# Kernel optimization log

Measured on AMD Instinct MI355X. Metric: run time of the kernel, lower is better.

## Reference

```python
import jax, jax.numpy as jnp
import numpy as np

B, S, E, H = 4, 2048, 1024, 16
D = E // H  # head_dim = 64


def setup_inputs() -> dict:
    key = jax.random.key(0)
    k1, k2, k3 = jax.random.split(key, 3)
    x = jax.random.normal(k1, (B, S, E), dtype=jnp.float32)
    w_attn = jax.random.normal(k2, (E, 3 * E), dtype=jnp.float32) * (E ** -0.5)
    b_attn = jnp.zeros((3 * E,), dtype=jnp.float32)
    w_out = jax.random.normal(k3, (E, E), dtype=jnp.float32) * (E ** -0.5)
    b_out = jnp.zeros((E,), dtype=jnp.float32)
    return {"x": x, "w_attn": w_attn, "b_attn": b_attn, "w_out": w_out, "b_out": b_out}


def reference(x, w_attn, b_attn, w_out, b_out):
    b, s, e = x.shape
    qkv = x @ w_attn + b_attn                      # [b, s, 3e]
    q, k, v = jnp.split(qkv, 3, axis=2)
    q = q.reshape(b, s, H, D)
    k = k.reshape(b, s, H, D)
    v = v.reshape(b, s, H, D)
    energy = jnp.einsum('nqhd,nkhd->nhqk', q, k)   # [b, H, s, s]
    causal = jnp.tril(jnp.ones((s, s), dtype=bool))
    energy = jnp.where(causal, energy, -jnp.inf)
    scale = jnp.sqrt(jnp.float32(D))
    attn = jax.nn.softmax(energy / scale, axis=-1)  # dropout_rate=0.0 -> identity
    out = jnp.einsum('nhql,nlhd->nqhd', attn, v).reshape(b, s, e)
    return out @ w_out + b_out
```

## Files before the change

kernel.cpp:

```cpp
#include <hip/hip_runtime.h>

typedef short bf16x8 __attribute__((ext_vector_type(8)));
typedef float f32x4 __attribute__((ext_vector_type(4)));
typedef float f32x16 __attribute__((ext_vector_type(16)));
typedef float float4v __attribute__((ext_vector_type(4)));
typedef short short4v __attribute__((ext_vector_type(4)));
typedef unsigned uint2v __attribute__((ext_vector_type(2)));
typedef unsigned uint4v __attribute__((ext_vector_type(4)));

#define B_ 4
#define S_ 2048
#define E_ 1024
#define H_ 16
#define D_ 64
#define M_ (B_*S_)
#define N1_ (3*E_)

__device__ inline short f2bs(float f) {
    unsigned u = __builtin_bit_cast(unsigned, f);
    unsigned r = u + 0x7fffu + ((u >> 16) & 1u);
    return (short)(r >> 16);
}
__device__ inline float exp2a(float x) {
    float r; asm("v_exp_f32 %0, %1" : "=v"(r) : "v"(x)); return r;
}
__device__ inline unsigned cvtpk(float a, float b) {
    unsigned r; asm("v_cvt_pk_bf16_f32 %0, %1, %2" : "=v"(r) : "v"(a), "v"(b)); return r;
}

__device__ inline const __attribute__((address_space(1))) void* gas(const void* p) {
    return (const __attribute__((address_space(1))) void*)p;
}
__device__ inline __attribute__((address_space(3))) void* las(void* p) {
    return (__attribute__((address_space(3))) void*)p;
}

__global__ __launch_bounds__(256) void prologue(
    const float* __restrict__ x, short* __restrict__ Xbf,
    const float* __restrict__ w_attn, short* __restrict__ Wat,
    const float* __restrict__ w_out, short* __restrict__ Wot) {
    __shared__ float t[32][33];
    const int bid = blockIdx.x;
    const int tid = threadIdx.x;
    if (bid < 2048) {
        const int n = M_ * E_;
        const int stride = 2048 * 256 * 4;
        for (int i = (bid * 256 + tid) * 4; i < n; i += stride) {
            float4v v = *(const float4v*)&x[i];
            short4v o;
            o[0] = f2bs(v[0]); o[1] = f2bs(v[1]); o[2] = f2bs(v[2]); o[3] = f2bs(v[3]);
            *(short4v*)&Xbf[i] = o;
        }
    } else {
        const float* in;
        short* out;
        int rows, cols, bx, by;
        if (bid < 5120) {
            in = w_attn; out = Wat; rows = E_; cols = N1_;
            int b2 = bid - 2048;
            bx = (b2 % 96) * 32; by = (b2 / 96) * 32;
        } else {
            in = w_out; out = Wot; rows = E_; cols = E_;
            int b2 = bid - 5120;
            bx = (b2 & 31) * 32; by = (b2 >> 5) * 32;
        }
        const int tx = tid & 31, ty = tid >> 5;
#pragma unroll
        for (int i = 0; i < 4; ++i)
            t[ty + i * 8][tx] = in[(size_t)(by + ty + i * 8) * cols + bx + tx];
        __syncthreads();
#pragma unroll
        for (int i = 0; i < 4; ++i)
            out[(size_t)(bx + ty + i * 8) * rows + by + tx] = f2bs(t[tx][ty + i * 8]);
    }
}

#define VMW(n) asm volatile("s_waitcnt vmcnt(" #n ")" ::: "memory")
#define NOP_ ((void)0)

#define QKV_MFMA1(Q, AF) \
    _Pragma("unroll") for (int nf = 0; nf < 6; ++nf) { \
        acc[(Q)][nf] = __builtin_amdgcn_mfma_f32_16x16x32_bf16(AF[0], bfrag[nf][0], acc[(Q)][nf], 0, 0, 0); \
        acc[(Q)][nf] = __builtin_amdgcn_mfma_f32_16x16x32_bf16(AF[1], bfrag[nf][1], acc[(Q)][nf], 0, 0, 0); \
    }

#define QKV_PHASE2(QA, STAGE_STMT, WAITV) do { \
    bf16x8 afA[2], afB[2]; \
    const char* lA0 = lA + (QA) * 4096; \
    const char* lA1 = lA + ((QA) + 1) * 4096; \
    _Pragma("unroll") for (int ks = 0; ks < 2; ++ks) { \
        afA[ks] = *(const bf16x8*)(lA0 + li * 128 + ((ks * 64 + g * 16) ^ ((li & 7) << 4))); \
        afB[ks] = *(const bf16x8*)(lA1 + li * 128 + ((ks * 64 + g * 16) ^ ((li & 7) << 4))); \
    } \
    STAGE_STMT; \
    __builtin_amdgcn_s_barrier(); \
    asm volatile("s_waitcnt lgkmcnt(0)" ::: "memory"); \
    __builtin_amdgcn_sched_barrier(0); \
    __builtin_amdgcn_s_setprio(1); \
    QKV_MFMA1(QA, afA); \
    QKV_MFMA1((QA) + 1, afB); \
    __builtin_amdgcn_s_setprio(0); \
    WAITV; \
    __builtin_amdgcn_s_barrier(); \
} while (0)

__global__ __launch_bounds__(256, 2) void gemm_qkv(
    const short* __restrict__ A, const short* __restrict__ Bt,
    const float* __restrict__ bias,
    short* __restrict__ Qb, short* __restrict__ Kb, short* __restrict__ Vt) {
    __shared__ __attribute__((aligned(16))) short ldsA[2][8192];
    __shared__ __attribute__((aligned(16))) short ldsB[2][12288];
    const int tid = threadIdx.x;
    const int lane = tid & 63;
    const int wid = tid >> 6;
    const int li = lane & 15, g = lane >> 4;
    const int wr = wid >> 1, wc = wid & 1;
    const int Kdim = E_;
    const int NT = Kdim >> 6;

    const int id = blockIdx.x;
    const int swz = (id & 7) * 128 + (id >> 3);
    const int bx = swz & 15, by = swz >> 4;
    const int row0 = by * 128, col0 = bx * 192;

    const int lr8 = lane >> 3;
    const int cstage = (((lane & 7) ^ (lr8 & 7)) << 4);

    auto stageA = [&](int buf, int kt) {
#pragma unroll
        for (int Q = 0; Q < 4; ++Q) {
            int grow = (wid >> 1) * 64 + Q * 16 + (wid & 1) * 8 + lr8;
            const char* src = (const char*)A +
                ((size_t)(row0 + grow) * Kdim + kt * 64) * 2 + cstage;
            char* dst = (char*)&ldsA[buf][0] + Q * 4096 + wid * 1024;
            __builtin_amdgcn_global_load_lds(gas(src), las(dst), 16, 0, 0);
        }
    };
    auto stageB = [&](int buf, int kt) {
#pragma unroll
        for (int i = 0; i < 6; ++i) {
            int grow = i * 32 + wid * 8 + lr8;
            const char* src = (const char*)Bt +
                ((size_t)(col0 + grow) * Kdim + kt * 64) * 2 + cstage;
            char* dst = (char*)&ldsB[buf][0] + i * 4096 + wid * 1024;
            __builtin_amdgcn_global_load_lds(gas(src), las(dst), 16, 0, 0);
        }
    };

    f32x4 acc[4][6];
#pragma unroll
    for (int m = 0; m < 4; ++m)
#pragma unroll
        for (int n = 0; n < 6; ++n) acc[m][n] = (f32x4){0.f, 0.f, 0.f, 0.f};

    stageB(0, 0);
    stageA(0, 0);
    asm volatile("s_waitcnt vmcnt(0)" ::: "memory");
    __syncthreads();

    for (int t = 0; t < NT; ++t) {
        const int cur = t & 1;
        const int nb = cur ^ 1;
        const int tn = t + 1;
        const bool st = (tn < NT);
        const char* lA = (const char*)&ldsA[cur][0] + wr * 2048;
        const char* lB = (const char*)&ldsB[cur][0];

        bf16x8 bfrag[6][2];
#pragma unroll
        for (int nf = 0; nf < 6; ++nf)
#pragma unroll
            for (int ks = 0; ks < 2; ++ks) {
                int r = wc * 96 + nf * 16 + li;
                bfrag[nf][ks] = *(const bf16x8*)(lB + r * 128 + ((ks * 64 + g * 16) ^ ((r & 7) << 4)));
            }
        if (st) {
            QKV_PHASE2(0, stageB(nb, tn), VMW(6));
            QKV_PHASE2(2, stageA(nb, tn), VMW(2));
        } else {
            QKV_PHASE2(0, NOP_, VMW(0));
            QKV_PHASE2(2, NOP_, NOP_);
        }
    }

#pragma unroll
    for (int nf = 0; nf < 6; ++nf) {
        int ncolg = col0 + wc * 96 + nf * 16 + li;
        float bv = bias[ncolg];
        int part = ncolg >> 10;
        int rem = ncolg & 1023;
        if (part < 2) {
            short* Dst = (part == 0) ? Qb : Kb;
#pragma unroll
            for (int mi = 0; mi < 4; ++mi) {
                int rbase = row0 + wr * 64 + mi * 16 + 4 * g;
#pragma unroll
                for (int j = 0; j < 4; ++j)
                    Dst[(size_t)(rbase + j) * E_ + rem] = f2bs(acc[mi][nf][j] + bv);
            }
        } else {
            int h = rem >> 6, d = rem & 63;
#pragma unroll
            for (int mi = 0; mi < 4; ++mi) {
                int s0 = row0 + wr * 64 + mi * 16 + 4 * g;
                int bb2 = s0 >> 11;
                int ss = s0 & 2047;
                uint2v p;
                p[0] = cvtpk(acc[mi][nf][0] + bv, acc[mi][nf][1] + bv);
                p[1] = cvtpk(acc[mi][nf][2] + bv, acc[mi][nf][3] + bv);
                *(uint2v*)&Vt[((size_t)(bb2 * H_ + h) * D_ + d) * S_ + ss] = p;
            }
        }
    }
}

#define OUT_MFMA1(Q, AF) \
    _Pragma("unroll") for (int nf = 0; nf < 4; ++nf) { \
        acc[(Q)][nf] = __builtin_amdgcn_mfma_f32_16x16x32_bf16(AF[0], bfrag[nf][0], acc[(Q)][nf], 0, 0, 0); \
        acc[(Q)][nf] = __builtin_amdgcn_mfma_f32_16x16x32_bf16(AF[1], bfrag[nf][1], acc[(Q)][nf], 0, 0, 0); \
    }

#define OUT_PHASE2(QA, STAGE_STMT, WAITV) do { \
    bf16x8 afA[2], afB[2]; \
    const char* lA0 = lA + (QA) * 4096; \
    const char* lA1 = lA + ((QA) + 1) * 4096; \
    _Pragma("unroll") for (int ks = 0; ks < 2; ++ks) { \
        afA[ks] = *(const bf16x8*)(lA0 + li * 128 + ((ks * 64 + g * 16) ^ ((li & 7) << 4))); \
        afB[ks] = *(const bf16x8*)(lA1 + li * 128 + ((ks * 64 + g * 16) ^ ((li & 7) << 4))); \
    } \
    STAGE_STMT; \
    __builtin_amdgcn_s_barrier(); \
    asm volatile("s_waitcnt lgkmcnt(0)" ::: "memory"); \
    __builtin_amdgcn_sched_barrier(0); \
    __builtin_amdgcn_s_setprio(1); \
    OUT_MFMA1(QA, afA); \
    OUT_MFMA1((QA) + 1, afB); \
    __builtin_amdgcn_s_setprio(0); \
    WAITV; \
    __builtin_amdgcn_s_barrier(); \
} while (0)

__global__ __launch_bounds__(256, 2) void gemm_out(
    const short* __restrict__ A, const short* __restrict__ Bt,
    const float* __restrict__ bias, float* __restrict__ Cf) {
    __shared__ __attribute__((aligned(16))) short ldsA[2][8192];
    __shared__ __attribute__((aligned(16))) short ldsB[2][8192];
    const int tid = threadIdx.x;
    const int lane = tid & 63;
    const int wid = tid >> 6;
    const int li = lane & 15, g = lane >> 4;
    const int wr = wid >> 1, wc = wid & 1;
    const int Kdim = E_;
    const int NT = Kdim >> 6;

    const int id = blockIdx.x;
    const int swz = (id & 7) * 64 + (id >> 3);
    const int bx = swz & 7, by = swz >> 3;
    const int row0 = by * 128, col0 = bx * 128;

    const int lr8 = lane >> 3;
    const int cstage = (((lane & 7) ^ (lr8 & 7)) << 4);

    auto stageA = [&](int buf, int kt) {
#pragma unroll
        for (int Q = 0; Q < 4; ++Q) {
            int grow = (wid >> 1) * 64 + Q * 16 + (wid & 1) * 8 + lr8;
            const char* src = (const char*)A +
                ((size_t)(row0 + grow) * Kdim + kt * 64) * 2 + cstage;
            char* dst = (char*)&ldsA[buf][0] + Q * 4096 + wid * 1024;
            __builtin_amdgcn_global_load_lds(gas(src), las(dst), 16, 0, 0);
        }
    };
    auto stageB = [&](int buf, int kt) {
#pragma unroll
        for (int i = 0; i < 4; ++i) {
            int grow = i * 32 + wid * 8 + lr8;
            const char* src = (const char*)Bt +
                ((size_t)(col0 + grow) * Kdim + kt * 64) * 2 + cstage;
            char* dst = (char*)&ldsB[buf][0] + i * 4096 + wid * 1024;
            __builtin_amdgcn_global_load_lds(gas(src), las(dst), 16, 0, 0);
        }
    };

    f32x4 acc[4][4];
#pragma unroll
    for (int m = 0; m < 4; ++m)
#pragma unroll
        for (int n = 0; n < 4; ++n) acc[m][n] = (f32x4){0.f, 0.f, 0.f, 0.f};

    stageB(0, 0);
    stageA(0, 0);
    asm volatile("s_waitcnt vmcnt(0)" ::: "memory");
    __syncthreads();

    for (int t = 0; t < NT; ++t) {
        const int cur = t & 1;
        const int nb = cur ^ 1;
        const int tn = t + 1;
        const bool st = (tn < NT);
        const char* lA = (const char*)&ldsA[cur][0] + wr * 2048;
        const char* lB = (const char*)&ldsB[cur][0];

        bf16x8 bfrag[4][2];
#pragma unroll
        for (int nf = 0; nf < 4; ++nf)
#pragma unroll
            for (int ks = 0; ks < 2; ++ks) {
                int r = wc * 64 + nf * 16 + li;
                bfrag[nf][ks] = *(const bf16x8*)(lB + r * 128 + ((ks * 64 + g * 16) ^ ((r & 7) << 4)));
            }
        if (st) {
            OUT_PHASE2(0, stageB(nb, tn), VMW(4));
            OUT_PHASE2(2, stageA(nb, tn), VMW(2));
        } else {
            OUT_PHASE2(0, NOP_, VMW(0));
            OUT_PHASE2(2, NOP_, NOP_);
        }
    }

#pragma unroll
    for (int nf = 0; nf < 4; ++nf) {
        int ncol = col0 + wc * 64 + nf * 16 + li;
        float bv = bias[ncol];
#pragma unroll
        for (int mi = 0; mi < 4; ++mi) {
            int rbase = row0 + wr * 64 + mi * 16 + 4 * g;
#pragma unroll
            for (int j = 0; j < 4; ++j)
                Cf[(size_t)(rbase + j) * E_ + ncol] = acc[mi][nf][j] + bv;
        }
    }
}

#define GRP 1040
__global__ __launch_bounds__(256, 4) void attn_kernel(
    const short* __restrict__ Qb, const short* __restrict__ Kb,
    const short* __restrict__ Vt, short* __restrict__ Ob) {
    __shared__ __attribute__((aligned(16))) char Kl[8 * GRP];
    __shared__ __attribute__((aligned(16))) char Vl[8 * GRP];
    const int lane = threadIdx.x & 63;
    const int wv = threadIdx.x >> 6;
    const int l31 = lane & 31;
    const int hi = lane >> 5;
    const int id = blockIdx.x;
    const int xcd = id & 7;
    const int r_ = id >> 3;
    const int qt = 15 - (r_ >> 3);
    const int bh = xcd * 8 + (r_ & 7);
    const int bb = bh >> 4, hh = bh & 15;
    const short* Qh = Qb + (size_t)bb * (S_ * E_) + hh * 64;
    const short* Kh = Kb + (size_t)bb * (S_ * E_) + hh * 64;
    const short* Vh = Vt + (size_t)bh * (D_ * S_);
    const float CEXP = 0.18033688011112042f;

    const int rstage = wv * 8 + (lane >> 3);
    const int cstage = (((lane & 7) ^ ((lane >> 3) & 7)) << 4);

    const int q0w = qt * 128 + wv * 32;
    const int q = q0w + l31;

    bf16x8 qf[4];
#pragma unroll
    for (int c = 0; c < 4; ++c)
        qf[c] = *(const bf16x8*)&Qh[(size_t)q * E_ + c * 16 + hi * 8];

    f32x16 acc[2];
#pragma unroll
    for (int d = 0; d < 2; ++d)
#pragma unroll
        for (int r = 0; r < 16; ++r) acc[d][r] = 0.f;
    float m = -3e38f, mC = 0.f, l = 0.f;

    const int nw = (q0w + 95) >> 6;
    const int nt = (qt * 128 + 191) >> 6;

    const int kg0 = (l31 >> 3) * GRP + (l31 & 7) * 128;
    const int kg1 = ((32 + l31) >> 3) * GRP + (l31 & 7) * 128;
    const int ksw = (l31 & 7) << 4;

    for (int it = 0; it < nt; ++it) {
        const int kt0 = it * 64;
#pragma unroll
        for (int half = 0; half < 2; ++half) {
            const int grp = half * 4 + wv;
            const char* gk = (const char*)(Kh + (size_t)(kt0 + half * 32 + rstage) * E_) + cstage;
            __builtin_amdgcn_global_load_lds(gas(gk), las(Kl + grp * GRP), 16, 0, 0);
            const char* gv = (const char*)Vh + (size_t)(half * 32 + rstage) * (S_ * 2) + (size_t)kt0 * 2 + cstage;
            __builtin_amdgcn_global_load_lds(gas(gv), las(Vl + grp * GRP), 16, 0, 0);
        }
        __syncthreads();
        if (it < nw) {
            f32x16 sc0, sc1;
#pragma unroll
            for (int r = 0; r < 16; ++r) { sc0[r] = 0.f; sc1[r] = 0.f; }
#pragma unroll
            for (int c = 0; c < 4; ++c) {
                bf16x8 kf0 = *(const bf16x8*)(Kl + kg0 + ((c * 32 + hi * 16) ^ ksw));
                bf16x8 kf1 = *(const bf16x8*)(Kl + kg1 + ((c * 32 + hi * 16) ^ ksw));
                sc0 = __builtin_amdgcn_mfma_f32_32x32x16_bf16(kf0, qf[c], sc0, 0, 0, 0);
                sc1 = __builtin_amdgcn_mfma_f32_32x32x16_bf16(kf1, qf[c], sc1, 0, 0, 0);
            }
            if (kt0 + 63 > q0w) {
                const int kb = kt0 + 4 * hi;
#pragma unroll
                for (int r = 0; r < 16; ++r) {
                    int key = kb + (r & 3) + 8 * (r >> 2);
                    sc0[r] = (key > q) ? -3e38f : sc0[r];
                    sc1[r] = (key + 32 > q) ? -3e38f : sc1[r];
                }
            }
            float tmx[8];
#pragma unroll
            for (int r = 0; r < 8; ++r)
                tmx[r] = fmaxf(fmaxf(sc0[2 * r], sc0[2 * r + 1]),
                               fmaxf(sc1[2 * r], sc1[2 * r + 1]));
            float tm = fmaxf(fmaxf(fmaxf(tmx[0], tmx[1]), fmaxf(tmx[2], tmx[3])),
                             fmaxf(fmaxf(tmx[4], tmx[5]), fmaxf(tmx[6], tmx[7])));
            tm = fmaxf(tm, __shfl_xor(tm, 32, 64));
            bool need = (tm > m + 16.0f);
            if (__ballot((int)need) != 0ull) {
                float mn = fmaxf(m, tm);
                float sf = exp2a((m - mn) * CEXP);
                m = mn; mC = mn * CEXP;
                l *= sf;
#pragma unroll
                for (int d = 0; d < 2; ++d)
#pragma unroll
                    for (int r = 0; r < 16; ++r) acc[d][r] *= sf;
            }
#pragma unroll
            for (int r = 0; r < 16; ++r) {
                sc0[r] = exp2a(fmaf(sc0[r], CEXP, -mC));
                sc1[r] = exp2a(fmaf(sc1[r], CEXP, -mC));
            }
            float s0 = 0.f, s1 = 0.f;
#pragma unroll
            for (int r = 0; r < 8; ++r) {
                s0 += sc0[2 * r] + sc0[2 * r + 1];
                s1 += sc1[2 * r] + sc1[2 * r + 1];
            }
            float ls = s0 + s1;
            ls += __shfl_xor(ls, 32, 64);
            l += ls;
            bf16x8 pf[4];
#pragma unroll
            for (int s = 0; s < 2; ++s) {
                const f32x16& p = s ? sc1 : sc0;
                unsigned a0 = cvtpk(p[0], p[1]),   a1 = cvtpk(p[2], p[3]);
                unsigned b0 = cvtpk(p[4], p[5]),   b1 = cvtpk(p[6], p[7]);
                unsigned a2 = cvtpk(p[8], p[9]),   a3 = cvtpk(p[10], p[11]);
                unsigned b2 = cvtpk(p[12], p[13]), b3 = cvtpk(p[14], p[15]);
                asm volatile("v_permlane32_swap_b32 %0, %1" : "+v"(a0), "+v"(b0));
                asm volatile("v_permlane32_swap_b32 %0, %1" : "+v"(a1), "+v"(b1));
                asm volatile("v_permlane32_swap_b32 %0, %1" : "+v"(a2), "+v"(b2));
                asm volatile("v_permlane32_swap_b32 %0, %1" : "+v"(a3), "+v"(b3));
                uint4v u1, u2;
                u1[0] = a0; u1[1] = a1; u1[2] = b0; u1[3] = b1;
                u2[0] = a2; u2[1] = a3; u2[2] = b2; u2[3] = b3;
                pf[s * 2] = __builtin_bit_cast(bf16x8, u1);
                pf[s * 2 + 1] = __builtin_bit_cast(bf16x8, u2);
            }
#pragma unroll
            for (int db = 0; db < 2; ++db) {
                const int row = db * 32 + l31;
                const int rsw = (row & 7) << 4;
                const char* vrow = Vl + (row >> 3) * GRP + (row & 7) * 128;
                bf16x8 v0 = *(const bf16x8*)(vrow + ((hi * 16) ^ rsw));
                bf16x8 v1 = *(const bf16x8*)(vrow + ((32 + hi * 16) ^ rsw));
                bf16x8 v2 = *(const bf16x8*)(vrow + ((64 + hi * 16) ^ rsw));
                bf16x8 v3 = *(const bf16x8*)(vrow + ((96 + hi * 16) ^ rsw));
                acc[db] = __builtin_amdgcn_mfma_f32_32x32x16_bf16(v0, pf[0], acc[db], 0, 0, 0);
                acc[db] = __builtin_amdgcn_mfma_f32_32x32x16_bf16(v1, pf[1], acc[db], 0, 0, 0);
                acc[db] = __builtin_amdgcn_mfma_f32_32x32x16_bf16(v2, pf[2], acc[db], 0, 0, 0);
                acc[db] = __builtin_amdgcn_mfma_f32_32x32x16_bf16(v3, pf[3], acc[db], 0, 0, 0);
            }
        }
        __syncthreads();
    }

    float rl = __builtin_amdgcn_rcpf(l);
    short* orow = Ob + ((size_t)(bb * S_ + q)) * E_ + hh * 64;
#pragma unroll
    for (int db = 0; db < 2; ++db)
#pragma unroll
        for (int rb = 0; rb < 4; ++rb) {
            uint2v pk;
            pk[0] = cvtpk(acc[db][rb * 4 + 0] * rl, acc[db][rb * 4 + 1] * rl);
            pk[1] = cvtpk(acc[db][rb * 4 + 2] * rl, acc[db][rb * 4 + 3] * rl);
            *(uint2v*)&orow[db * 32 + rb * 8 + hi * 4] = pk;
        }
}

extern "C" void kernel_launch(void* const* d_in, const int* in_sizes, int n_in,
                              void* d_out, int out_size, void* d_ws, size_t ws_size,
                              hipStream_t stream) {
    const float* x      = (const float*)d_in[0];
    const float* w_attn = (const float*)d_in[1];
    const float* b_attn = (const float*)d_in[2];
    const float* w_out  = (const float*)d_in[3];
    const float* b_out  = (const float*)d_in[4];
    float* out = (float*)d_out;

    char* ws = (char*)d_ws;
    short* Xbf  = (short*)(ws);
    short* Wat  = (short*)(ws + (16ull << 20));
    short* Wot  = (short*)(ws + (22ull << 20));
    short* Qb   = (short*)(ws + (24ull << 20));
    short* Kb   = (short*)(ws + (40ull << 20));
    short* Vt   = (short*)(ws + (56ull << 20));
    short* Obuf = Xbf;

    prologue<<<6144, 256, 0, stream>>>(x, Xbf, w_attn, Wat, w_out, Wot);

    gemm_qkv<<<1024, 256, 0, stream>>>(Xbf, Wat, b_attn, Qb, Kb, Vt);

    attn_kernel<<<1024, 256, 0, stream>>>(Qb, Kb, Vt, Obuf);

    gemm_out<<<512, 256, 0, stream>>>(Obuf, Wot, b_out, out);
}
```

Measured before the change: 151.4 us.

## Double-buffer K/V LDS tiles in attention kernel to overlap loads with compute

Splits the K and V shared-memory tiles into two buffers and issues the global-to-LDS loads for the next key tile before computing on the current one. The loop now waits on a partial vmcnt instead of draining all loads at the top of each iteration, so memory latency can hide behind the MFMA and softmax work. LDS use per block doubles (about 33 KB), which may lower occupancy under the 4-blocks-per-CU launch bound. The extra barriers and manual waitcnt also have to be correct for the asynchronous LDS writes.

```diff
diff --git a/kernel.cpp b/kernel.cpp
--- a/kernel.cpp
+++ b/kernel.cpp
@@ -336,8 +336,8 @@
 __global__ __launch_bounds__(256, 4) void attn_kernel(
     const short* __restrict__ Qb, const short* __restrict__ Kb,
     const short* __restrict__ Vt, short* __restrict__ Ob) {
-    __shared__ __attribute__((aligned(16))) char Kl[8 * GRP];
-    __shared__ __attribute__((aligned(16))) char Vl[8 * GRP];
+    __shared__ __attribute__((aligned(16))) char Kl[2][8 * GRP];
+    __shared__ __attribute__((aligned(16))) char Vl[2][8 * GRP];
     const int lane = threadIdx.x & 63;
     const int wv = threadIdx.x >> 6;
     const int l31 = lane & 31;
@@ -378,25 +378,41 @@
     const int kg1 = ((32 + l31) >> 3) * GRP + (l31 & 7) * 128;
     const int ksw = (l31 & 7) << 4;
 
-    for (int it = 0; it < nt; ++it) {
+    auto stage = [&](int it, int buf) {
         const int kt0 = it * 64;
 #pragma unroll
         for (int half = 0; half < 2; ++half) {
             const int grp = half * 4 + wv;
             const char* gk = (const char*)(Kh + (size_t)(kt0 + half * 32 + rstage) * E_) + cstage;
-            __builtin_amdgcn_global_load_lds(gas(gk), las(Kl + grp * GRP), 16, 0, 0);
+            __builtin_amdgcn_global_load_lds(gas(gk), las(&Kl[buf][0] + grp * GRP), 16, 0, 0);
             const char* gv = (const char*)Vh + (size_t)(half * 32 + rstage) * (S_ * 2) + (size_t)kt0 * 2 + cstage;
-            __builtin_amdgcn_global_load_lds(gas(gv), las(Vl + grp * GRP), 16, 0, 0);
-        }
-        __syncthreads();
+            __builtin_amdgcn_global_load_lds(gas(gv), las(&Vl[buf][0] + grp * GRP), 16, 0, 0);
+        }
+    };
+
+    stage(0, 0);
+
+    for (int it = 0; it < nt; ++it) {
+        const int buf = it & 1;
+        if (it + 1 < nt) {
+            stage(it + 1, buf ^ 1);
+            VMW(4);
+        } else {
+            VMW(0);
+        }
+        __builtin_amdgcn_s_barrier();
+        __builtin_amdgcn_sched_barrier(0);
         if (it < nw) {
+            const int kt0 = it * 64;
+            const char* Kb_ = &Kl[buf][0];
+            const char* Vb_ = &Vl[buf][0];
             f32x16 sc0, sc1;
 #pragma unroll
             for (int r = 0; r < 16; ++r) { sc0[r] = 0.f; sc1[r] = 0.f; }
 #pragma unroll
             for (int c = 0; c < 4; ++c) {
-                bf16x8 kf0 = *(const bf16x8*)(Kl + kg0 + ((c * 32 + hi * 16) ^ ksw));
-                bf16x8 kf1 = *(const bf16x8*)(Kl + kg1 + ((c * 32 + hi * 16) ^ ksw));
+                bf16x8 kf0 = *(const bf16x8*)(Kb_ + kg0 + ((c * 32 + hi * 16) ^ ksw));
+                bf16x8 kf1 = *(const bf16x8*)(Kb_ + kg1 + ((c * 32 + hi * 16) ^ ksw));
                 sc0 = __builtin_amdgcn_mfma_f32_32x32x16_bf16(kf0, qf[c], sc0, 0, 0, 0);
                 sc1 = __builtin_amdgcn_mfma_f32_32x32x16_bf16(kf1, qf[c], sc1, 0, 0, 0);
             }
@@ -464,7 +480,7 @@
             for (int db = 0; db < 2; ++db) {
                 const int row = db * 32 + l31;
                 const int rsw = (row & 7) << 4;
-                const char* vrow = Vl + (row >> 3) * GRP + (row & 7) * 128;
+                const char* vrow = Vb_ + (row >> 3) * GRP + (row & 7) * 128;
                 bf16x8 v0 = *(const bf16x8*)(vrow + ((hi * 16) ^ rsw));
                 bf16x8 v1 = *(const bf16x8*)(vrow + ((32 + hi * 16) ^ rsw));
                 bf16x8 v2 = *(const bf16x8*)(vrow + ((64 + hi * 16) ^ rsw));
@@ -475,7 +491,8 @@
                 acc[db] = __builtin_amdgcn_mfma_f32_32x32x16_bf16(v3, pf[3], acc[db], 0, 0, 0);
             }
         }
-        __syncthreads();
+        asm volatile("s_waitcnt lgkmcnt(0)" ::: "memory");
+        __builtin_amdgcn_s_barrier();
     }
 
     float rl = __builtin_amdgcn_rcpf(l);
```

Result: no change. 151.8 us, median of 2 (+0.3%).
